# Kernel optimization log

Hardware: AMD Instinct MI355X
Metric: run time of the kernel (lower is better)

The kernel has to match this reference:

```python
import jax, jax.numpy as jnp
import numpy as np

K = 5               # kernel size of the causal/dilated convs
N_LAYERS = 30       # params.n_dilation_conv_layers
CYCLE = 10          # n_dilation_conv_layers / n_dilation_cycles
MU = 255.0          # quantization_channels - 1 for mu-law expansion
B, T = 8, 262144


def dil_causal_conv(x, w, b, d):
    """Single-channel dilated causal conv. x:[B,1,T], w:[K], b:scalar/[1]."""
    P = (K - 1) * d
    xp = jnp.pad(x, ((0, 0), (0, 0), (P, 0)))
    Tn = x.shape[-1]
    # cross-correlation, matching torch Conv1d with left pad then right crop
    y = w[0] * xp[..., 0:Tn]
    for j in range(1, K):
        y = y + w[j] * xp[..., j * d: j * d + Tn]
    return y + b


def setup_inputs() -> dict:
    key = jax.random.key(0)
    ks = jax.random.split(key, 14)
    n = lambda k, shape, s=0.2: jax.random.normal(k, shape, dtype=jnp.float32) * s
    return {
        "x": jax.random.normal(ks[0], (B, 1, T), dtype=jnp.float32),
        "causal_w": n(ks[1], (K,)),
        "causal_b": n(ks[2], (1,)),
        "filter_w": n(ks[3], (N_LAYERS, K)),
        "filter_b": n(ks[4], (N_LAYERS,)),
        "gate_w": n(ks[5], (N_LAYERS, K)),
        "gate_b": n(ks[6], (N_LAYERS,)),
        "res_w": n(ks[7], (N_LAYERS,)),
        "res_b": n(ks[8], (N_LAYERS,)),
        "conv1_w": n(ks[9], (1,)),
        "conv1_b": n(ks[10], (1,)),
        "conv2_w": n(ks[11], (1,)),
        "conv2_b": n(ks[12], (1,)),
    }


def reference(x, causal_w, causal_b, filter_w, filter_b, gate_w, gate_b,
              res_w, res_b, conv1_w, conv1_b, conv2_w, conv2_b):
    dilations = [2 ** (k % CYCLE) for k in range(N_LAYERS)]
    h = dil_causal_conv(x, causal_w, causal_b, 1)
    skip = jnp.zeros_like(h)
    for k, d in enumerate(dilations):
        f = jnp.tanh(dil_causal_conv(h, filter_w[k], filter_b[k], d))
        g = jax.nn.sigmoid(dil_causal_conv(h, gate_w[k], gate_b[k], d))
        o = f * g                      # gated activation (skip output)
        h = res_w[k] * o + res_b[k] + h  # 1x1 residual conv + residual add
        skip = skip + o
    out = conv1_w * jax.nn.relu(skip) + conv1_b   # 1x1 conv
    out = conv2_w * jax.nn.relu(out) + conv2_b    # 1x1 conv
    # mu-law expanding, quantization_channels=256
    out = jnp.sign(out) * jnp.expm1(jnp.abs(out) * jnp.log1p(MU)) / MU
    return jax.nn.softmax(out, axis=-1)
```

## Files before the change

### kernel.cpp

```cpp
#include <hip/hip_runtime.h>

#define T_LEN 262144
#define B_SZ 8
#define CHUNK 8192
#define HALO 4096
#define NTHREADS 1024
#define NGROUPS ((CHUNK + HALO) / 4)
#define CHUNKS_PER_ROW (T_LEN / CHUNK)
#define NBLOCKS (B_SZ * CHUNKS_PER_ROW)
#define LOG2E 1.4426950408889634f
#define NEG2LOG2E (-2.8853900817779268f)
#define NEGLOG2E  (-1.4426950408889634f)

typedef float f32x2 __attribute__((ext_vector_type(2)));
typedef float f32x4 __attribute__((ext_vector_type(4)));
typedef _Float16 f16x2 __attribute__((ext_vector_type(2)));
typedef __fp16 fp16x2 __attribute__((ext_vector_type(2)));

__device__ __forceinline__ float frcp(float x)  { return __builtin_amdgcn_rcpf(x); }
__device__ __forceinline__ float fexp2(float x) { return __builtin_amdgcn_exp2f(x); }
__device__ __forceinline__ f32x2 pair(float s)  { f32x2 r = {s, s}; return r; }
__device__ __forceinline__ f32x2 lo2(f32x4 v)   { return __builtin_shufflevector(v, v, 0, 1); }
__device__ __forceinline__ f32x2 hi2(f32x4 v)   { return __builtin_shufflevector(v, v, 2, 3); }
__device__ __forceinline__ f32x4 cat4(f32x2 a, f32x2 b) {
    f32x4 r; r.x = a.x; r.y = a.y; r.z = b.x; r.w = b.y; return r;
}
__device__ __forceinline__ unsigned b32(f16x2 v) { return __builtin_bit_cast(unsigned, v); }
__device__ __forceinline__ f16x2 hbits(unsigned u) { return __builtin_bit_cast(f16x2, u); }
__device__ __forceinline__ f16x2 hsplat(float s) { _Float16 h = (_Float16)s; f16x2 r = {h, h}; return r; }
__device__ __forceinline__ f16x2 hfma(f16x2 a, f16x2 b, f16x2 c) { return __builtin_elementwise_fma(a, b, c); }
__device__ __forceinline__ f16x2 pkrtz(float x, float y) {
    fp16x2 t = __builtin_amdgcn_cvt_pkrtz(x, y);
    return __builtin_bit_cast(f16x2, t);
}
__device__ __forceinline__ f32x4 h2f4(f16x2 a, f16x2 b) {
    f32x2 lo = __builtin_convertvector(a, f32x2);
    f32x2 hi = __builtin_convertvector(b, f32x2);
    return cat4(lo, hi);
}

__device__ __forceinline__ f32x2 pkfma2(f32x2 a, f32x2 b, f32x2 c) {
    f32x2 d;
    asm("v_pk_fma_f32 %0, %1, %2, %3" : "=v"(d) : "v"(a), "v"(b), "v"(c));
    return d;
}
__device__ __forceinline__ f32x2 pkadd2(f32x2 a, f32x2 b) {
    f32x2 d;
    asm("v_pk_add_f32 %0, %1, %2" : "=v"(d) : "v"(a), "v"(b));
    return d;
}
__device__ __forceinline__ f32x2 pksub2(f32x2 a, f32x2 b) {
    f32x2 d;
    asm("v_pk_add_f32 %0, %1, %2 neg_lo:[0,1] neg_hi:[0,1]" : "=v"(d) : "v"(a), "v"(b));
    return d;
}
__device__ __forceinline__ f32x2 pkmul2(f32x2 a, f32x2 b) {
    f32x2 d;
    asm("v_pk_mul_f32 %0, %1, %2" : "=v"(d) : "v"(a), "v"(b));
    return d;
}
__device__ __forceinline__ f32x4 pfma_v(f32x4 a, f32x4 b, f32x4 c) {
    return cat4(pkfma2(lo2(a), lo2(b), lo2(c)), pkfma2(hi2(a), hi2(b), hi2(c)));
}
__device__ __forceinline__ f32x4 padd_s(f32x2 s, f32x4 b) {
    return cat4(pkadd2(s, lo2(b)), pkadd2(s, hi2(b)));
}
__device__ __forceinline__ f32x4 psub_s(f32x2 s, f32x4 b) {
    return cat4(pksub2(s, lo2(b)), pksub2(s, hi2(b)));
}
__device__ __forceinline__ f32x4 pmul_v(f32x4 a, f32x4 b) {
    return cat4(pkmul2(lo2(a), lo2(b)), pkmul2(hi2(a), hi2(b)));
}

__device__ __forceinline__ f32x4 gate4(f32x4 af, f32x4 ag, f32x2 one) {
    f32x4 E1, E2, rc;
    E1.x = fexp2(af.x); E1.y = fexp2(af.y); E1.z = fexp2(af.z); E1.w = fexp2(af.w);
    E2.x = fexp2(ag.x); E2.y = fexp2(ag.y); E2.z = fexp2(ag.z); E2.w = fexp2(ag.w);
    f32x4 d1  = padd_s(one, E1);
    f32x4 den = pfma_v(E2, d1, d1);
    f32x4 num = psub_s(one, E1);
    rc.x = frcp(den.x); rc.y = frcp(den.y); rc.z = frcp(den.z); rc.w = frcp(den.w);
    return pmul_v(num, rc);
}
__device__ __forceinline__ float mulaw(float v, float c1wv, float c1bv, float c2wv, float c2bv) {
    float a  = __builtin_fmaf(c1wv, fmaxf(v, 0.0f), c1bv);
    float b2 = __builtin_fmaf(c2wv, fmaxf(a, 0.0f), c2bv);
    float m  = fexp2(fabsf(b2) * 8.0f) - 1.0f;
    return copysignf(m * (1.0f / 255.0f), b2);
}

template <int STAGE>
__global__ __launch_bounds__(NTHREADS, 4)
void stage_kernel(const void* __restrict__ in_,
                  const float* __restrict__ cw, const float* __restrict__ cb,
                  const float* __restrict__ fw, const float* __restrict__ fb,
                  const float* __restrict__ gw, const float* __restrict__ gb,
                  const float* __restrict__ rw, const float* __restrict__ rb,
                  uint2* __restrict__ hout, uint2* __restrict__ skbuf,
                  uint2* __restrict__ pout,
                  const float* __restrict__ c1w, const float* __restrict__ c1b,
                  const float* __restrict__ c2w, const float* __restrict__ c2b,
                  float2* __restrict__ blockstats)
{
    __shared__ uint2 bufl[2][NGROUPS];
    __shared__ float red[NTHREADS / 64];

    const int tid = threadIdx.x;
    const int bid = blockIdx.x;
    const int row = bid / CHUNKS_PER_ROW;
    const int chunk = bid % CHUNKS_PER_ROW;
    const int rowbase = row * T_LEN;
    const int base_t = chunk * CHUNK;
    const bool first = (chunk == 0);
    const f16x2 HZ = hsplat(0.0f);

    f16x2 hA[3], hB[3];
    if (STAGE == 0) {
        const float* inb = (const float*)in_ + rowbase + base_t - HALO;
        #pragma unroll
        for (int w = 0; w < 3; ++w) {
            int G = tid + w * NTHREADS;
            if (w == 0 && first) { hA[w] = HZ; hB[w] = HZ; }
            else {
                f32x4 v = *(const f32x4*)(inb + 4 * G);
                hA[w] = pkrtz(v.x, v.y);
                hB[w] = pkrtz(v.z, v.w);
            }
            bufl[0][G] = make_uint2(b32(hA[w]), b32(hB[w]));
        }
    } else {
        const uint2* inb = (const uint2*)in_ + ((rowbase + base_t - HALO) >> 2);
        #pragma unroll
        for (int w = 0; w < 3; ++w) {
            int G = tid + w * NTHREADS;
            uint2 u = (w == 0 && first) ? make_uint2(0u, 0u) : inb[G];
            bufl[0][G] = u;
            hA[w] = hbits(u.x); hB[w] = hbits(u.y);
        }
    }
    f16x2 s1A, s1B, s2A, s2B;
    const int skb = ((rowbase + base_t) >> 2) + tid;
    if (STAGE == 0) { s1A = HZ; s1B = HZ; s2A = HZ; s2B = HZ; }
    else {
        uint2 u1 = skbuf[skb], u2 = skbuf[skb + 1024];
        s1A = hbits(u1.x); s1B = hbits(u1.y);
        s2A = hbits(u2.x); s2B = hbits(u2.y);
    }
    __syncthreads();

    const f32x2 ONE = pair(1.0f);

    if (STAGE == 0) {
        const f16x2 C0 = hsplat(cw[4]), C1 = hsplat(cw[3]), C2 = hsplat(cw[2]),
                    C3 = hsplat(cw[1]), C4 = hsplat(cw[0]), BB = hsplat(cb[0]);
        #pragma unroll
        for (int w = 0; w < 3; ++w) {
            int G = tid + w * NTHREADS;
            int gm = G - 1; if (w == 0) gm = gm < 0 ? 0 : gm;
            uint2 P = bufl[0][gm];
            unsigned uA = b32(hA[w]), uB = b32(hB[w]);
            unsigned t1A = __builtin_amdgcn_perm(uA, P.y, 0x05040302u);
            unsigned t1B = __builtin_amdgcn_perm(uB, uA, 0x05040302u);
            unsigned t3A = __builtin_amdgcn_perm(P.y, P.x, 0x05040302u);
            f16x2 aA = hfma(C0, hA[w], BB);
            f16x2 aB = hfma(C0, hB[w], BB);
            aA = hfma(C1, hbits(t1A), aA); aB = hfma(C1, hbits(t1B), aB);
            aA = hfma(C2, hbits(P.y), aA); aB = hfma(C2, hbits(uA), aB);
            aA = hfma(C3, hbits(t3A), aA); aB = hfma(C3, hbits(t1A), aB);
            aA = hfma(C4, hbits(P.x), aA); aB = hfma(C4, hbits(P.y), aB);
            if (w == 0 && first) { aA = HZ; aB = HZ; }
            hA[w] = aA; hB[w] = aB;
            bufl[1][G] = make_uint2(b32(aA), b32(aB));
        }
        __syncthreads();
    }

    #pragma unroll
    for (int k = 0; k < 10; ++k) {
        const int c = (STAGE == 0) ? ((k + 1) & 1) : (k & 1);
        const int d = 1 << k;
        const int L = STAGE * 10 + k;
        const float* fwL = fw + 5 * L;
        const float* gwL = gw + 5 * L;
        const f16x2 WF0 = hsplat(fwL[4] * NEG2LOG2E), WF1 = hsplat(fwL[3] * NEG2LOG2E),
                    WF2 = hsplat(fwL[2] * NEG2LOG2E), WF3 = hsplat(fwL[1] * NEG2LOG2E),
                    WF4 = hsplat(fwL[0] * NEG2LOG2E);
        const f16x2 WG0 = hsplat(gwL[4] * NEGLOG2E), WG1 = hsplat(gwL[3] * NEGLOG2E),
                    WG2 = hsplat(gwL[2] * NEGLOG2E), WG3 = hsplat(gwL[1] * NEGLOG2E),
                    WG4 = hsplat(gwL[0] * NEGLOG2E);
        const f16x2 FB = hsplat(fb[L] * NEG2LOG2E), GB = hsplat(gb[L] * NEGLOG2E);
        const f16x2 RW = hsplat(rw[L]), RB = hsplat(rb[L]);
        const uint2* __restrict__ bufc = bufl[c];
        uint2* __restrict__ bufd = bufl[c ^ 1];

        #pragma unroll
        for (int w = 0; w < 3; ++w) {
            const int G = tid + w * NTHREADS;
            if (w == 0 && tid < (2 << k)) continue;
            f16x2 cA = hA[w], cB = hB[w];
            f16x2 t1a, t1b, t2a, t2b, t3a, t3b, t4a, t4b;
            if (d >= 4) {
                const int DG = d >> 2;
                const uint2* bp = bufc + (G - 4 * DG);
                uint2 U4 = bp[0], U3 = bp[DG], U2 = bp[2 * DG], U1 = bp[3 * DG];
                t1a = hbits(U1.x); t1b = hbits(U1.y);
                t2a = hbits(U2.x); t2b = hbits(U2.y);
                t3a = hbits(U3.x); t3b = hbits(U3.y);
                t4a = hbits(U4.x); t4b = hbits(U4.y);
            } else if (d == 1) {
                uint2 P = bufc[G - 1];
                unsigned uA = b32(cA);
                unsigned w1A = __builtin_amdgcn_perm(uA, P.y, 0x05040302u);
                unsigned w1B = __builtin_amdgcn_perm(b32(cB), uA, 0x05040302u);
                unsigned w3A = __builtin_amdgcn_perm(P.y, P.x, 0x05040302u);
                t1a = hbits(w1A); t1b = hbits(w1B);
                t2a = hbits(P.y); t2b = cA;
                t3a = hbits(w3A); t3b = hbits(w1A);
                t4a = hbits(P.x); t4b = hbits(P.y);
            } else {
                uint2 P = bufc[G - 1], Q = bufc[G - 2];
                t1a = hbits(P.y); t1b = cA;
                t2a = hbits(P.x); t2b = hbits(P.y);
                t3a = hbits(Q.y); t3b = hbits(P.x);
                t4a = hbits(Q.x); t4b = hbits(Q.y);
            }
            f16x2 afA = hfma(WF0, cA, FB), afB = hfma(WF0, cB, FB);
            afA = hfma(WF1, t1a, afA); afB = hfma(WF1, t1b, afB);
            afA = hfma(WF2, t2a, afA); afB = hfma(WF2, t2b, afB);
            afA = hfma(WF3, t3a, afA); afB = hfma(WF3, t3b, afB);
            afA = hfma(WF4, t4a, afA); afB = hfma(WF4, t4b, afB);
            f16x2 agA = hfma(WG0, cA, GB), agB = hfma(WG0, cB, GB);
            agA = hfma(WG1, t1a, agA); agB = hfma(WG1, t1b, agB);
            agA = hfma(WG2, t2a, agA); agB = hfma(WG2, t2b, agB);
            agA = hfma(WG3, t3a, agA); agB = hfma(WG3, t3b, agB);
            agA = hfma(WG4, t4a, agA); agB = hfma(WG4, t4b, agB);
            f32x4 o = gate4(h2f4(afA, afB), h2f4(agA, agB), ONE);
            f16x2 oA = pkrtz(o.x, o.y), oB = pkrtz(o.z, o.w);
            f16x2 nA = hfma(RW, oA, cA + RB);
            f16x2 nB = hfma(RW, oB, cB + RB);
            if (w == 0 && first) { nA = HZ; nB = HZ; }
            hA[w] = nA; hB[w] = nB;
            if (k < 9) bufd[G] = make_uint2(b32(nA), b32(nB));
            if (w == 1) { s1A = s1A + oA; s1B = s1B + oB; }
            if (w == 2) { s2A = s2A + oA; s2B = s2B + oB; }
        }
        if (k < 9) __syncthreads();
    }

    if (STAGE < 2) {
        uint2* hp = hout + ((rowbase + base_t) >> 2);
        hp[tid]        = make_uint2(b32(hA[1]), b32(hB[1]));
        hp[tid + 1024] = make_uint2(b32(hA[2]), b32(hB[2]));
        skbuf[skb]        = make_uint2(b32(s1A), b32(s1B));
        skbuf[skb + 1024] = make_uint2(b32(s2A), b32(s2B));
    } else {
        const float c1wv = c1w[0], c1bv = c1b[0], c2wv = c2w[0], c2bv = c2b[0];
        f32x4 sk1 = h2f4(s1A, s1B), sk2 = h2f4(s2A, s2B);
        f32x4 p1, p2;
        p1.x = mulaw(sk1.x, c1wv, c1bv, c2wv, c2bv);
        p1.y = mulaw(sk1.y, c1wv, c1bv, c2wv, c2bv);
        p1.z = mulaw(sk1.z, c1wv, c1bv, c2wv, c2bv);
        p1.w = mulaw(sk1.w, c1wv, c1bv, c2wv, c2bv);
        p2.x = mulaw(sk2.x, c1wv, c1bv, c2wv, c2bv);
        p2.y = mulaw(sk2.y, c1wv, c1bv, c2wv, c2bv);
        p2.z = mulaw(sk2.z, c1wv, c1bv, c2wv, c2bv);
        p2.w = mulaw(sk2.w, c1wv, c1bv, c2wv, c2bv);
        f16x2 q1A = pkrtz(p1.x, p1.y), q1B = pkrtz(p1.z, p1.w);
        f16x2 q2A = pkrtz(p2.x, p2.y), q2B = pkrtz(p2.z, p2.w);
        pout[skb]        = make_uint2(b32(q1A), b32(q1B));
        pout[skb + 1024] = make_uint2(b32(q2A), b32(q2B));
        p1 = h2f4(q1A, q1B);
        p2 = h2f4(q2A, q2B);

        float pmax = fmaxf(fmaxf(fmaxf(p1.x, p1.y), fmaxf(p1.z, p1.w)),
                           fmaxf(fmaxf(p2.x, p2.y), fmaxf(p2.z, p2.w)));
        #pragma unroll
        for (int off = 32; off; off >>= 1) pmax = fmaxf(pmax, __shfl_xor(pmax, off, 64));
        if ((tid & 63) == 0) red[tid >> 6] = pmax;
        __syncthreads();
        float bmax = red[0];
        #pragma unroll
        for (int i = 1; i < NTHREADS / 64; ++i) bmax = fmaxf(bmax, red[i]);
        __syncthreads();

        float ps = fexp2((p1.x - bmax) * LOG2E) + fexp2((p1.y - bmax) * LOG2E)
                 + fexp2((p1.z - bmax) * LOG2E) + fexp2((p1.w - bmax) * LOG2E)
                 + fexp2((p2.x - bmax) * LOG2E) + fexp2((p2.y - bmax) * LOG2E)
                 + fexp2((p2.z - bmax) * LOG2E) + fexp2((p2.w - bmax) * LOG2E);
        #pragma unroll
        for (int off = 32; off; off >>= 1) ps += __shfl_xor(ps, off, 64);
        if ((tid & 63) == 0) red[tid >> 6] = ps;
        __syncthreads();
        if (tid == 0) {
            float s = 0.0f;
            #pragma unroll
            for (int i = 0; i < NTHREADS / 64; ++i) s += red[i];
            blockstats[bid] = make_float2(bmax, s);
        }
    }
}

__global__ __launch_bounds__(NTHREADS)
void norm_kernel(const uint2* __restrict__ p16, const float2* __restrict__ bs,
                 float* __restrict__ out)
{
    const int tid = threadIdx.x, bid = blockIdx.x;
    const int row = bid / CHUNKS_PER_ROW;
    float m = -3.0e38f;
    #pragma unroll
    for (int j = 0; j < CHUNKS_PER_ROW; ++j)
        m = fmaxf(m, bs[row * CHUNKS_PER_ROW + j].x);
    float cc = 0.0f;
    #pragma unroll
    for (int j = 0; j < CHUNKS_PER_ROW; ++j) {
        float2 v = bs[row * CHUNKS_PER_ROW + j];
        cc += v.y * fexp2((v.x - m) * LOG2E);
    }
    const float inv = 1.0f / cc;
    const int base4 = ((row * T_LEN + (bid % CHUNKS_PER_ROW) * CHUNK) >> 2) + tid;
    #pragma unroll
    for (int part = 0; part < 2; ++part) {
        uint2 u = p16[base4 + part * NTHREADS];
        f32x4 v = h2f4(hbits(u.x), hbits(u.y));
        f32x4 q;
        q.x = fexp2((v.x - m) * LOG2E) * inv;
        q.y = fexp2((v.y - m) * LOG2E) * inv;
        q.z = fexp2((v.z - m) * LOG2E) * inv;
        q.w = fexp2((v.w - m) * LOG2E) * inv;
        *(f32x4*)(out + 4 * (base4 + part * NTHREADS)) = q;
    }
}

extern "C" void kernel_launch(void* const* d_in, const int* in_sizes, int n_in,
                              void* d_out, int out_size, void* d_ws, size_t ws_size,
                              hipStream_t stream)
{
    (void)in_sizes; (void)n_in; (void)out_size; (void)ws_size;
    const float* x   = (const float*)d_in[0];
    const float* cw  = (const float*)d_in[1];
    const float* cb  = (const float*)d_in[2];
    const float* fw  = (const float*)d_in[3];
    const float* fb  = (const float*)d_in[4];
    const float* gw  = (const float*)d_in[5];
    const float* gb  = (const float*)d_in[6];
    const float* rw  = (const float*)d_in[7];
    const float* rb  = (const float*)d_in[8];
    const float* c1w = (const float*)d_in[9];
    const float* c1b = (const float*)d_in[10];
    const float* c2w = (const float*)d_in[11];
    const float* c2b = (const float*)d_in[12];
    float* out = (float*)d_out;

    const size_t NTOT = (size_t)B_SZ * T_LEN;
    uint2*  hA = (uint2*)d_ws;
    uint2*  hB = (uint2*)((char*)d_ws + 2 * NTOT);
    uint2*  sk = (uint2*)((char*)d_ws + 4 * NTOT);
    float2* bs = (float2*)((char*)d_ws + 6 * NTOT);

    stage_kernel<0><<<NBLOCKS, NTHREADS, 0, stream>>>(x,  cw, cb, fw, fb, gw, gb, rw, rb,
                                                      hA, sk, nullptr, c1w, c1b, c2w, c2b, bs);
    stage_kernel<1><<<NBLOCKS, NTHREADS, 0, stream>>>(hA, cw, cb, fw, fb, gw, gb, rw, rb,
                                                      hB, sk, nullptr, c1w, c1b, c2w, c2b, bs);
    stage_kernel<2><<<NBLOCKS, NTHREADS, 0, stream>>>(hB, cw, cb, fw, fb, gw, gb, rw, rb,
                                                      nullptr, sk, hA, c1w, c1b, c2w, c2b, bs);
    norm_kernel<<<NBLOCKS, NTHREADS, 0, stream>>>(hA, bs, out);
}
```

Baseline: 74.35 us.

## Fuse softmax normalization into final stage via per-row atomic barrier

Removes the separate norm kernel and the fp16 intermediate buffer of mu-law outputs. Each block of the last stage publishes its partial max/sum, increments a per-row counter, spins until all 32 chunks of its row are done, then normalizes its values in registers and writes the output directly. This saves a kernel launch and a round trip through global memory. It relies on all 256 blocks being co-resident (no forward-progress guarantee otherwise), which risks deadlock, and the spin-wait adds latency.

```diff
diff --git a/kernel.cpp b/kernel.cpp
--- a/kernel.cpp
+++ b/kernel.cpp
@@ -97,10 +97,10 @@
                   const float* __restrict__ gw, const float* __restrict__ gb,
                   const float* __restrict__ rw, const float* __restrict__ rb,
                   uint2* __restrict__ hout, uint2* __restrict__ skbuf,
-                  uint2* __restrict__ pout,
                   const float* __restrict__ c1w, const float* __restrict__ c1b,
                   const float* __restrict__ c2w, const float* __restrict__ c2b,
-                  float2* __restrict__ blockstats)
+                  float2* __restrict__ bs, unsigned* __restrict__ rowcnt,
+                  float* __restrict__ out)
 {
     __shared__ uint2 bufl[2][NGROUPS];
     __shared__ float red[NTHREADS / 64];
@@ -113,6 +113,8 @@
     const int base_t = chunk * CHUNK;
     const bool first = (chunk == 0);
     const f16x2 HZ = hsplat(0.0f);
+
+    if (STAGE == 0 && bid == 0 && tid < B_SZ) rowcnt[tid] = 0u;
 
     f16x2 hA[3], hB[3];
     if (STAGE == 0) {
@@ -265,12 +267,6 @@
         p2.y = mulaw(sk2.y, c1wv, c1bv, c2wv, c2bv);
         p2.z = mulaw(sk2.z, c1wv, c1bv, c2wv, c2bv);
         p2.w = mulaw(sk2.w, c1wv, c1bv, c2wv, c2bv);
-        f16x2 q1A = pkrtz(p1.x, p1.y), q1B = pkrtz(p1.z, p1.w);
-        f16x2 q2A = pkrtz(p2.x, p2.y), q2B = pkrtz(p2.z, p2.w);
-        pout[skb]        = make_uint2(b32(q1A), b32(q1B));
-        pout[skb + 1024] = make_uint2(b32(q2A), b32(q2B));
-        p1 = h2f4(q1A, q1B);
-        p2 = h2f4(q2A, q2B);
 
         float pmax = fmaxf(fmaxf(fmaxf(p1.x, p1.y), fmaxf(p1.z, p1.w)),
                            fmaxf(fmaxf(p2.x, p2.y), fmaxf(p2.z, p2.w)));
@@ -291,43 +287,43 @@
         for (int off = 32; off; off >>= 1) ps += __shfl_xor(ps, off, 64);
         if ((tid & 63) == 0) red[tid >> 6] = ps;
         __syncthreads();
+
         if (tid == 0) {
             float s = 0.0f;
             #pragma unroll
             for (int i = 0; i < NTHREADS / 64; ++i) s += red[i];
-            blockstats[bid] = make_float2(bmax, s);
-        }
-    }
-}
-
-__global__ __launch_bounds__(NTHREADS)
-void norm_kernel(const uint2* __restrict__ p16, const float2* __restrict__ bs,
-                 float* __restrict__ out)
-{
-    const int tid = threadIdx.x, bid = blockIdx.x;
-    const int row = bid / CHUNKS_PER_ROW;
-    float m = -3.0e38f;
-    #pragma unroll
-    for (int j = 0; j < CHUNKS_PER_ROW; ++j)
-        m = fmaxf(m, bs[row * CHUNKS_PER_ROW + j].x);
-    float cc = 0.0f;
-    #pragma unroll
-    for (int j = 0; j < CHUNKS_PER_ROW; ++j) {
-        float2 v = bs[row * CHUNKS_PER_ROW + j];
-        cc += v.y * fexp2((v.x - m) * LOG2E);
-    }
-    const float inv = 1.0f / cc;
-    const int base4 = ((row * T_LEN + (bid % CHUNKS_PER_ROW) * CHUNK) >> 2) + tid;
-    #pragma unroll
-    for (int part = 0; part < 2; ++part) {
-        uint2 u = p16[base4 + part * NTHREADS];
-        f32x4 v = h2f4(hbits(u.x), hbits(u.y));
-        f32x4 q;
-        q.x = fexp2((v.x - m) * LOG2E) * inv;
-        q.y = fexp2((v.y - m) * LOG2E) * inv;
-        q.z = fexp2((v.z - m) * LOG2E) * inv;
-        q.w = fexp2((v.w - m) * LOG2E) * inv;
-        *(f32x4*)(out + 4 * (base4 + part * NTHREADS)) = q;
+            bs[bid] = make_float2(bmax, s);
+            __threadfence();
+            atomicAdd(&rowcnt[row], 1u);
+            while (atomicAdd(&rowcnt[row], 0u) < (unsigned)CHUNKS_PER_ROW)
+                __builtin_amdgcn_s_sleep(2);
+            __threadfence();
+        }
+        __syncthreads();
+
+        float m = -3.0e38f;
+        #pragma unroll
+        for (int j = 0; j < CHUNKS_PER_ROW; ++j)
+            m = fmaxf(m, bs[row * CHUNKS_PER_ROW + j].x);
+        float cc = 0.0f;
+        #pragma unroll
+        for (int j = 0; j < CHUNKS_PER_ROW; ++j) {
+            float2 v = bs[row * CHUNKS_PER_ROW + j];
+            cc += v.y * fexp2((v.x - m) * LOG2E);
+        }
+        const float inv = 1.0f / cc;
+
+        f32x4 q1, q2;
+        q1.x = fexp2((p1.x - m) * LOG2E) * inv;
+        q1.y = fexp2((p1.y - m) * LOG2E) * inv;
+        q1.z = fexp2((p1.z - m) * LOG2E) * inv;
+        q1.w = fexp2((p1.w - m) * LOG2E) * inv;
+        q2.x = fexp2((p2.x - m) * LOG2E) * inv;
+        q2.y = fexp2((p2.y - m) * LOG2E) * inv;
+        q2.z = fexp2((p2.z - m) * LOG2E) * inv;
+        q2.w = fexp2((p2.w - m) * LOG2E) * inv;
+        *(f32x4*)(out + rowbase + base_t + 4 * tid)        = q1;
+        *(f32x4*)(out + rowbase + base_t + 4096 + 4 * tid) = q2;
     }
 }
 
@@ -352,16 +348,19 @@
     float* out = (float*)d_out;
 
     const size_t NTOT = (size_t)B_SZ * T_LEN;
-    uint2*  hA = (uint2*)d_ws;
-    uint2*  hB = (uint2*)((char*)d_ws + 2 * NTOT);
-    uint2*  sk = (uint2*)((char*)d_ws + 4 * NTOT);
-    float2* bs = (float2*)((char*)d_ws + 6 * NTOT);
+    uint2*    hA = (uint2*)d_ws;
+    uint2*    hB = (uint2*)((char*)d_ws + 2 * NTOT);
+    uint2*    sk = (uint2*)((char*)d_ws + 4 * NTOT);
+    float2*   bs = (float2*)((char*)d_ws + 6 * NTOT);
+    unsigned* rowcnt = (unsigned*)((char*)d_ws + 6 * NTOT + 4096);
 
     stage_kernel<0><<<NBLOCKS, NTHREADS, 0, stream>>>(x,  cw, cb, fw, fb, gw, gb, rw, rb,
-                                                      hA, sk, nullptr, c1w, c1b, c2w, c2b, bs);
+                                                      hA, sk, c1w, c1b, c2w, c2b,
+                                                      bs, rowcnt, out);
     stage_kernel<1><<<NBLOCKS, NTHREADS, 0, stream>>>(hA, cw, cb, fw, fb, gw, gb, rw, rb,
-                                                      hB, sk, nullptr, c1w, c1b, c2w, c2b, bs);
+                                                      hB, sk, c1w, c1b, c2w, c2b,
+                                                      bs, rowcnt, out);
     stage_kernel<2><<<NBLOCKS, NTHREADS, 0, stream>>>(hB, cw, cb, fw, fb, gw, gb, rw, rb,
-                                                      nullptr, sk, hA, c1w, c1b, c2w, c2b, bs);
-    norm_kernel<<<NBLOCKS, NTHREADS, 0, stream>>>(hA, bs, out);
-}
+                                                      nullptr, sk, c1w, c1b, c2w, c2b,
+                                                      bs, rowcnt, out);
+}
```

Result: slower. 86.03 us (+15.7%).
